# Optimization experiments

Hardware: AMD Instinct MI355X
Metric: run time of the kernel (lower is better)

Reference implementation:

```python
import jax, jax.numpy as jnp
import numpy as np
from jax import lax

GROUPS = 8
THR = 0.5
EPS = 1e-5

def setup_inputs() -> dict:
    key = jax.random.key(0)
    ks = jax.random.split(key, 7)
    b, c, h, w = 64, 256, 1024, 1
    cg = c // GROUPS  # 32
    x = jax.random.normal(ks[0], (b, c, h, w), jnp.float32)
    w1 = jax.random.normal(ks[1], (cg, cg), jnp.float32) * 0.1     # conv1x1 weight [out,in]
    b1 = jnp.zeros((cg,), jnp.float32)
    w3 = jax.random.normal(ks[2], (cg, cg, 3, 3), jnp.float32) * 0.05  # conv3x3 OIHW
    b3 = jnp.zeros((cg,), jnp.float32)
    gamma = jnp.ones((cg,), jnp.float32)
    beta = jnp.zeros((cg,), jnp.float32)
    return {"x": x, "w1": w1, "b1": b1, "w3": w3, "b3": b3, "gamma": gamma, "beta": beta}

def reference(x, w1, b1, w3, b3, gamma, beta):
    b, c, h, w = x.shape
    g = GROUPS
    cg = c // g
    bg = b * g
    gx = x.reshape(bg, cg, h, w)

    # pool_h is AvgPool2d((1,1)) -> identity; pool_w averages over h then permutes
    x_h = gx                                               # [bg,cg,h,1]
    x_w = jnp.mean(gx, axis=2, keepdims=True).transpose(0, 1, 3, 2)  # [bg,cg,w,1]
    cat = jnp.concatenate([x_h, x_w], axis=2)              # [bg,cg,h+w,1]
    hw = jnp.einsum('oi,bihw->bohw', w1, cat) + b1[None, :, None, None]
    xh, xw = hw[:, :, :h], hw[:, :, h:]                    # [bg,cg,h,1], [bg,cg,w,1]

    gated = gx * jax.nn.sigmoid(xh) * jax.nn.sigmoid(xw.transpose(0, 1, 3, 2))
    # GroupNorm(cg, cg): normalize each channel over spatial dims, affine per channel
    mu = jnp.mean(gated, axis=(2, 3), keepdims=True)
    var = jnp.mean(jnp.square(gated - mu), axis=(2, 3), keepdims=True)
    x1 = (gated - mu) * lax.rsqrt(var + EPS) * gamma[None, :, None, None] + beta[None, :, None, None]

    x2 = lax.conv_general_dilated(gx, w3, (1, 1), ((1, 1), (1, 1)),
                                  dimension_numbers=('NCHW', 'OIHW', 'NCHW')) + b3[None, :, None, None]

    # agp: AvgPool2d((avg_len,1)) with h==avg_len, w==1 -> mean over spatial dims
    x11 = jax.nn.softmax(jnp.mean(x1, axis=(2, 3)), axis=-1)  # [bg,cg]
    x21 = jax.nn.softmax(jnp.mean(x2, axis=(2, 3)), axis=-1)  # [bg,cg]
    x12 = x2.reshape(bg, cg, h * w)
    x22 = x1.reshape(bg, cg, h * w)
    weights = (jnp.einsum('bc,bcn->bn', x11, x12) +
               jnp.einsum('bc,bcn->bn', x21, x22)).reshape(bg, 1, h, w)

    rew = gx * jax.nn.sigmoid(weights)
    info = rew >= THR
    x_1 = jnp.where(info, gx, 0.0)
    x_2 = jnp.where(info, 0.0, gx)
    half = cg // 2
    out = jnp.concatenate([x_1[:, :half] + x_2[:, half:],
                           x_1[:, half:] + x_2[:, :half]], axis=1)
    return out.reshape(b, c, h, w)
```

## Files before the change

### kernel.cpp

```cpp
#include <hip/hip_runtime.h>
#include <math.h>

#define CG   32
#define H    1024
#define NBG  512
#define CHN  8
#define BROW (H + 2)
#define EPSV 1e-5f
#define THRV 0.5f

__global__ __launch_bounds__(1024)
__attribute__((amdgpu_waves_per_eu(4, 4)))
void emaru_kernel(const float* __restrict__ x,  const float* __restrict__ w1,
                  const float* __restrict__ b1, const float* __restrict__ w3,
                  const float* __restrict__ b3, const float* __restrict__ gamma,
                  const float* __restrict__ beta, float* __restrict__ out)
{
    __shared__ float  buf[CHN][BROW];
    __shared__ float  w1s[1024];
    __shared__ float  w3s[3072];
    __shared__ double sumS[CG];
    __shared__ float  sigwS[CG], x11S[CG], x21S[CG], As[CG], Bs[CG], Cs[CG],
                      muS[CG], rsgS[CG], b1S[CG], b3S[CG], betaS[CG],
                      g0S[CG], gNS[CG], gammaS[CG];

    const int t  = threadIdx.x;
    const int bg = blockIdx.x;
    const long base = (long)bg * (CG * H);
    const int wid = t >> 6, lane = t & 63;

    w1s[t] = w1[t];
    #pragma unroll
    for (int r = 0; r < 3; ++r) w3s[r*1024 + t] = w3[(r*1024 + t)*3 + 1];
    if (t < CG) { b1S[t] = b1[t]; b3S[t] = b3[t]; betaS[t] = beta[t]; gammaS[t] = gamma[t]; }

    float g[CG];
    #pragma unroll
    for (int c = 0; c < CG; ++c) g[c] = x[base + c*H + t];
    if (t == 0) {
        #pragma unroll
        for (int c = 0; c < CG; ++c) g0S[c] = g[c];
    }
    if (t == H-1) {
        #pragma unroll
        for (int c = 0; c < CG; ++c) gNS[c] = g[c];
    }
    __syncthreads();

    if (t < CG) {
        float m = betaS[0];
        #pragma unroll
        for (int i = 1; i < CG; ++i) m = fmaxf(m, betaS[i]);
        float s = 0.f;
        #pragma unroll
        for (int i = 0; i < CG; ++i) s += expf(betaS[i] - m);
        const float inv = 1.f / s;
        x11S[t] = expf(betaS[t] - m) * inv;
        float a = 0.f, b = 0.f, c = 0.f;
        #pragma unroll
        for (int o = 0; o < CG; ++o) {
            const float f = expf(betaS[o] - m) * inv;
            a = fmaf(f, w3s[(o*CG + t)*3 + 0], a);
            b = fmaf(f, w3s[(o*CG + t)*3 + 1], b);
            c = fmaf(f, w3s[(o*CG + t)*3 + 2], c);
        }
        As[t] = a; Bs[t] = b; Cs[t] = c;
    }

    float cd = 0.f;
    #pragma unroll
    for (int ch = 0; ch < CG/CHN; ++ch) {
        __syncthreads();
        #pragma unroll
        for (int i = 0; i < CHN; ++i) buf[i][1 + t] = g[ch*CHN + i];
        if (t < CHN) { buf[t][0] = 0.f; buf[t][1 + H] = 0.f; }
        __syncthreads();
        if (wid < CHN) {
            double acc = 0.0;
            #pragma unroll
            for (int k = 0; k < 16; ++k) acc += (double)buf[wid][1 + lane + (k << 6)];
            #pragma unroll
            for (int off = 32; off; off >>= 1) acc += __shfl_down(acc, off);
            if (lane == 0) sumS[ch*CHN + wid] = acc;
        }
        #pragma unroll
        for (int i = 0; i < CHN; ++i) {
            const int gi = ch*CHN + i;
            cd = fmaf(As[gi], buf[i][t],     cd);
            cd = fmaf(Bs[gi], g[gi],         cd);
            cd = fmaf(Cs[gi], buf[i][2 + t], cd);
        }
    }
    __syncthreads();

    if (wid == 0 && lane < CG) {
        const int o = lane;
        float acc = b1S[o];
        for (int i = 0; i < CG; ++i) {
            const float mi = (float)(sumS[i] * (1.0/H));
            acc = fmaf(w1s[o*CG + i], mi, acc);
        }
        sigwS[o] = 1.f / (1.f + expf(-acc));
    } else if (wid == 1 && lane < CG) {
        const int o = lane;
        double m2 = 0.0;
        for (int i = 0; i < CG; ++i) {
            const double Si = sumS[i];
            m2 += (double)w3s[(o*CG + i)*3 + 0] * (Si - (double)gNS[i])
                + (double)w3s[(o*CG + i)*3 + 1] * Si
                + (double)w3s[(o*CG + i)*3 + 2] * (Si - (double)g0S[i]);
        }
        float mv = (float)(m2 * (1.0/H)) + b3S[o];
        float mx = mv;
        #pragma unroll
        for (int off = 16; off; off >>= 1) mx = fmaxf(mx, __shfl_xor(mx, off));
        const float e = expf(mv - mx);
        float se = e;
        #pragma unroll
        for (int off = 16; off; off >>= 1) se += __shfl_xor(se, off);
        x21S[o] = e / se;
    }
    __syncthreads();

    #pragma unroll
    for (int o = 0; o < CG; ++o) cd = fmaf(x11S[o], b3S[o], cd);
    float wsum = cd;
    #pragma unroll
    for (int ch = 0; ch < CG/CHN; ++ch) {
        __syncthreads();
        #pragma unroll
        for (int i = 0; i < CHN; ++i) {
            const int o = ch*CHN + i;
            float acc = b1S[o];
            #pragma unroll
            for (int i4 = 0; i4 < CG/4; ++i4) {
                const float4 wv = *reinterpret_cast<const float4*>(&w1s[o*CG + i4*4]);
                acc = fmaf(wv.x, g[i4*4+0], acc);
                acc = fmaf(wv.y, g[i4*4+1], acc);
                acc = fmaf(wv.z, g[i4*4+2], acc);
                acc = fmaf(wv.w, g[i4*4+3], acc);
            }
            buf[i][1 + t] = g[o] * (1.f / (1.f + expf(-acc))) * sigwS[o];
        }
        __syncthreads();
        if (wid < CHN) {
            double sg = 0.0, sq = 0.0;
            #pragma unroll
            for (int k = 0; k < 16; ++k) {
                const double v = (double)buf[wid][1 + lane + (k << 6)];
                sg += v; sq = fma(v, v, sq);
            }
            #pragma unroll
            for (int off = 32; off; off >>= 1) { sg += __shfl_down(sg, off); sq += __shfl_down(sq, off); }
            if (lane == 0) {
                const int o = ch*CHN + wid;
                const double mu  = sg * (1.0/H);
                const double var = sq * (1.0/H) - mu*mu;
                muS[o]  = (float)mu;
                rsgS[o] = (float)(1.0 / sqrt(var + (double)EPSV)) * gammaS[o];
            }
        }
        __syncthreads();
        #pragma unroll
        for (int i = 0; i < CHN; ++i) {
            const int o = ch*CHN + i;
            const float x1o = fmaf(buf[i][1 + t] - muS[o], rsgS[o], betaS[o]);
            wsum = fmaf(x21S[o], x1o, wsum);
        }
    }

    const float s = 1.f / (1.f + expf(-wsum));
    #pragma unroll
    for (int o = 0; o < CG/2; ++o) {
        const float ga = g[o], gb = g[o + CG/2];
        const bool ia = (ga * s) >= THRV;
        const bool ib = (gb * s) >= THRV;
        out[base + o*H + t]          = (ia ? ga : 0.f) + (ib ? 0.f : gb);
        out[base + (o + CG/2)*H + t] = (ib ? gb : 0.f) + (ia ? 0.f : ga);
    }
}

extern "C" void kernel_launch(void* const* d_in, const int* in_sizes, int n_in,
                              void* d_out, int out_size, void* d_ws, size_t ws_size,
                              hipStream_t stream) {
    const float* x     = (const float*)d_in[0];
    const float* w1    = (const float*)d_in[1];
    const float* b1    = (const float*)d_in[2];
    const float* w3    = (const float*)d_in[3];
    const float* b3    = (const float*)d_in[4];
    const float* gamma = (const float*)d_in[5];
    const float* beta  = (const float*)d_in[6];
    float* out = (float*)d_out;
    emaru_kernel<<<NBG, 1024, 0, stream>>>(x, w1, b1, w3, b3, gamma, beta, out);
}
```

Baseline: 396.7 us.

## Drop per-thread channel register cache and re-read input from global memory

Removes the 32-element per-thread register array holding the group's input and instead re-loads x from global memory at each stage, computing the 1x1 gate conv as a per-channel outer-product accumulation into 8 outputs. It also removes the fixed waves-per-EU attribute. The intent is to cut register pressure and raise occupancy, at the cost of several extra passes over the input that rely on cache hits.

```diff
diff --git a/kernel.cpp b/kernel.cpp
--- a/kernel.cpp
+++ b/kernel.cpp
@@ -10,7 +10,6 @@
 #define THRV 0.5f
 
 __global__ __launch_bounds__(1024)
-__attribute__((amdgpu_waves_per_eu(4, 4)))
 void emaru_kernel(const float* __restrict__ x,  const float* __restrict__ w1,
                   const float* __restrict__ b1, const float* __restrict__ w3,
                   const float* __restrict__ b3, const float* __restrict__ gamma,
@@ -25,26 +24,13 @@
                       g0S[CG], gNS[CG], gammaS[CG];
 
     const int t  = threadIdx.x;
-    const int bg = blockIdx.x;
-    const long base = (long)bg * (CG * H);
+    const long base = (long)blockIdx.x * (CG * H);
     const int wid = t >> 6, lane = t & 63;
 
     w1s[t] = w1[t];
     #pragma unroll
     for (int r = 0; r < 3; ++r) w3s[r*1024 + t] = w3[(r*1024 + t)*3 + 1];
     if (t < CG) { b1S[t] = b1[t]; b3S[t] = b3[t]; betaS[t] = beta[t]; gammaS[t] = gamma[t]; }
-
-    float g[CG];
-    #pragma unroll
-    for (int c = 0; c < CG; ++c) g[c] = x[base + c*H + t];
-    if (t == 0) {
-        #pragma unroll
-        for (int c = 0; c < CG; ++c) g0S[c] = g[c];
-    }
-    if (t == H-1) {
-        #pragma unroll
-        for (int c = 0; c < CG; ++c) gNS[c] = g[c];
-    }
     __syncthreads();
 
     if (t < CG) {
@@ -72,7 +58,7 @@
     for (int ch = 0; ch < CG/CHN; ++ch) {
         __syncthreads();
         #pragma unroll
-        for (int i = 0; i < CHN; ++i) buf[i][1 + t] = g[ch*CHN + i];
+        for (int i = 0; i < CHN; ++i) buf[i][1 + t] = x[base + (ch*CHN + i)*H + t];
         if (t < CHN) { buf[t][0] = 0.f; buf[t][1 + H] = 0.f; }
         __syncthreads();
         if (wid < CHN) {
@@ -83,11 +69,12 @@
             for (int off = 32; off; off >>= 1) acc += __shfl_down(acc, off);
             if (lane == 0) sumS[ch*CHN + wid] = acc;
         }
+        if (t < CHN) { g0S[ch*CHN + t] = buf[t][1]; gNS[ch*CHN + t] = buf[t][H]; }
         #pragma unroll
         for (int i = 0; i < CHN; ++i) {
             const int gi = ch*CHN + i;
             cd = fmaf(As[gi], buf[i][t],     cd);
-            cd = fmaf(Bs[gi], g[gi],         cd);
+            cd = fmaf(Bs[gi], buf[i][1 + t], cd);
             cd = fmaf(Cs[gi], buf[i][2 + t], cd);
         }
     }
@@ -126,21 +113,22 @@
     for (int o = 0; o < CG; ++o) cd = fmaf(x11S[o], b3S[o], cd);
     float wsum = cd;
     #pragma unroll
-    for (int ch = 0; ch < CG/CHN; ++ch) {
+    for (int oc = 0; oc < CG/CHN; ++oc) {
         __syncthreads();
+        float acc[CHN];
         #pragma unroll
-        for (int i = 0; i < CHN; ++i) {
-            const int o = ch*CHN + i;
-            float acc = b1S[o];
+        for (int j = 0; j < CHN; ++j) acc[j] = b1S[oc*CHN + j];
+        for (int i = 0; i < CG; ++i) {
+            const float xi = x[base + i*H + t];
             #pragma unroll
-            for (int i4 = 0; i4 < CG/4; ++i4) {
-                const float4 wv = *reinterpret_cast<const float4*>(&w1s[o*CG + i4*4]);
-                acc = fmaf(wv.x, g[i4*4+0], acc);
-                acc = fmaf(wv.y, g[i4*4+1], acc);
-                acc = fmaf(wv.z, g[i4*4+2], acc);
-                acc = fmaf(wv.w, g[i4*4+3], acc);
-            }
-            buf[i][1 + t] = g[o] * (1.f / (1.f + expf(-acc))) * sigwS[o];
+            for (int j = 0; j < CHN; ++j)
+                acc[j] = fmaf(w1s[(oc*CHN + j)*CG + i], xi, acc[j]);
+        }
+        #pragma unroll
+        for (int j = 0; j < CHN; ++j) {
+            const int o = oc*CHN + j;
+            const float gj = x[base + o*H + t];
+            buf[j][1 + t] = gj * (1.f / (1.f + expf(-acc[j]))) * sigwS[o];
         }
         __syncthreads();
         if (wid < CHN) {
@@ -153,7 +141,7 @@
             #pragma unroll
             for (int off = 32; off; off >>= 1) { sg += __shfl_down(sg, off); sq += __shfl_down(sq, off); }
             if (lane == 0) {
-                const int o = ch*CHN + wid;
+                const int o = oc*CHN + wid;
                 const double mu  = sg * (1.0/H);
                 const double var = sq * (1.0/H) - mu*mu;
                 muS[o]  = (float)mu;
@@ -162,9 +150,9 @@
         }
         __syncthreads();
         #pragma unroll
-        for (int i = 0; i < CHN; ++i) {
-            const int o = ch*CHN + i;
-            const float x1o = fmaf(buf[i][1 + t] - muS[o], rsgS[o], betaS[o]);
+        for (int j = 0; j < CHN; ++j) {
+            const int o = oc*CHN + j;
+            const float x1o = fmaf(buf[j][1 + t] - muS[o], rsgS[o], betaS[o]);
             wsum = fmaf(x21S[o], x1o, wsum);
         }
     }
@@ -172,11 +160,12 @@
     const float s = 1.f / (1.f + expf(-wsum));
     #pragma unroll
     for (int o = 0; o < CG/2; ++o) {
-        const float ga = g[o], gb = g[o + CG/2];
+        const float ga = x[base + o*H + t];
+        const float gb = x[base + (o + CG/2)*H + t];
         const bool ia = (ga * s) >= THRV;
         const bool ib = (gb * s) >= THRV;
-        out[base + o*H + t]          = (ia ? ga : 0.f) + (ib ? 0.f : gb);
-        out[base + (o + CG/2)*H + t] = (ib ? gb : 0.f) + (ia ? 0.f : ga);
+        out[base + o*H + t]            = (ia ? ga : 0.f) + (ib ? 0.f : gb);
+        out[base + (o + CG/2)*H + t]   = (ib ? gb : 0.f) + (ia ? 0.f : ga);
     }
 }
 
```

Result: slower. 488.9 us (+23.2%).
